# Kernel optimization log

Measured on AMD Instinct MI355X. Metric: run time of the kernel, lower is better.

## Reference

```python
import jax, jax.numpy as jnp
import numpy as np
import math

POOL_OUT = 64  # AdaptiveAvgPool1d output_size


def setup_inputs() -> dict:
    key = jax.random.key(0)
    k1, k2 = jax.random.split(key)
    B, L, C = 8, 4096, 2048
    M, P = 4, 512  # masks per image, num_sample_point
    input_feats = jax.random.normal(k1, (B, L, C), dtype=jnp.float32)
    # normalized (y, x) point coords in [0,1), as produced by m.nonzero()/img_wh
    points_yx = jax.random.uniform(k2, (B, M, P, 2), dtype=jnp.float32)
    return {"input_feats": input_feats, "points_yx": points_yx}


def _point_sample_pool(input_feats, points_yx):
    B, L, C = input_feats.shape
    H = W = int(math.isqrt(L))  # feat.reshape(h, w, c) with h = w = sqrt(L)
    _, M, P, _ = points_yx.shape
    feat = input_feats.reshape(B, H, W, C)

    # point_sample: grid = 2*p - 1, grid_sample align_corners=True =>
    # pixel coord = (grid+1)/2*(dim-1) = p*(dim-1)
    iy = points_yx[..., 0] * (H - 1)  # [B,M,P]
    ix = points_yx[..., 1] * (W - 1)
    y0f = jnp.floor(iy)
    x0f = jnp.floor(ix)
    wy = (iy - y0f)[..., None]  # [B,M,P,1]
    wx = (ix - x0f)[..., None]
    y0 = jnp.clip(y0f.astype(jnp.int32), 0, H - 1)
    x0 = jnp.clip(x0f.astype(jnp.int32), 0, W - 1)
    y1 = jnp.clip(y0 + 1, 0, H - 1)
    x1 = jnp.clip(x0 + 1, 0, W - 1)

    flat = feat.reshape(B, H * W, C)

    def gather(yi, xi):
        idx = (yi * W + xi).reshape(B, M * P)
        return jnp.take_along_axis(flat, idx[..., None], axis=1).reshape(B, M, P, C)

    f00 = gather(y0, x0)
    f01 = gather(y0, x1)
    f10 = gather(y1, x0)
    f11 = gather(y1, x1)
    sampled = (f00 * (1 - wx) + f01 * wx) * (1 - wy) + (f10 * (1 - wx) + f11 * wx) * wy

    # AdaptiveAvgPool1d(output_size=POOL_OUT) over point dim; P % POOL_OUT == 0
    # so it reduces to a chunked mean.
    k = P // POOL_OUT
    pooled = sampled.reshape(B, M, POOL_OUT, k, C).mean(axis=3)
    return pooled  # [B, M, POOL_OUT, C]


def reference(input_feats, points_yx):
    return _point_sample_pool(input_feats, points_yx)
```

## Files before the change

kernel.cpp:

```cpp
#include <hip/hip_runtime.h>

constexpr int Bc    = 8;
constexpr int Lc    = 4096;
constexpr int Cc    = 2048;
constexpr int Mc    = 4;
constexpr int Pc    = 512;
constexpr int POOLc = 64;
constexpr int Kc    = 8;
constexpr int Hc    = 64;
constexpr int Wc    = 64;

__device__ __forceinline__ void fma4(float4& acc, float w, const float4 v) {
    acc.x = fmaf(w, v.x, acc.x);
    acc.y = fmaf(w, v.y, acc.y);
    acc.z = fmaf(w, v.z, acc.z);
    acc.w = fmaf(w, v.w, acc.w);
}

__global__ __launch_bounds__(256) void point_sample_pool_kernel(
    const float* __restrict__ feats,
    const float* __restrict__ pts,
    float* __restrict__ out)
{
    const int blk = blockIdx.x;
    const int o   = blk & (POOLc - 1);
    const int bm  = blk >> 6;
    const int b   = bm >> 2;
    const int tid = threadIdx.x;

    const int cA = tid * 4;
    const int cB = cA + (Cc / 2);

    const float* fb = feats + (size_t)b * Lc * Cc;
    const float* pb = pts + ((size_t)bm * Pc + (size_t)o * Kc) * 2;

    float4 accA = make_float4(0.f, 0.f, 0.f, 0.f);
    float4 accB = make_float4(0.f, 0.f, 0.f, 0.f);

#pragma unroll
    for (int j = 0; j < Kc; ++j) {
        const float py = pb[2 * j + 0];
        const float px = pb[2 * j + 1];
        const float iy = py * (float)(Hc - 1);
        const float ix = px * (float)(Wc - 1);
        const float y0f = floorf(iy);
        const float x0f = floorf(ix);
        const float wy = iy - y0f;
        const float wx = ix - x0f;
        int y0 = (int)y0f; y0 = y0 < 0 ? 0 : (y0 > Hc - 1 ? Hc - 1 : y0);
        int x0 = (int)x0f; x0 = x0 < 0 ? 0 : (x0 > Wc - 1 ? Wc - 1 : x0);
        const int y1 = (y0 + 1 > Hc - 1) ? Hc - 1 : y0 + 1;
        const int x1 = (x0 + 1 > Wc - 1) ? Wc - 1 : x0 + 1;

        const float w00 = (1.f - wx) * (1.f - wy);
        const float w01 = wx * (1.f - wy);
        const float w10 = (1.f - wx) * wy;
        const float w11 = wx * wy;

        const float* r00 = fb + (size_t)(y0 * Wc + x0) * Cc;
        const float* r01 = fb + (size_t)(y0 * Wc + x1) * Cc;
        const float* r10 = fb + (size_t)(y1 * Wc + x0) * Cc;
        const float* r11 = fb + (size_t)(y1 * Wc + x1) * Cc;

        const float4 a00 = *(const float4*)(r00 + cA);
        const float4 b00 = *(const float4*)(r00 + cB);
        const float4 a01 = *(const float4*)(r01 + cA);
        const float4 b01 = *(const float4*)(r01 + cB);
        const float4 a10 = *(const float4*)(r10 + cA);
        const float4 b10 = *(const float4*)(r10 + cB);
        const float4 a11 = *(const float4*)(r11 + cA);
        const float4 b11 = *(const float4*)(r11 + cB);

        fma4(accA, w00, a00); fma4(accB, w00, b00);
        fma4(accA, w01, a01); fma4(accB, w01, b01);
        fma4(accA, w10, a10); fma4(accB, w10, b10);
        fma4(accA, w11, a11); fma4(accB, w11, b11);
    }

    const float inv_k = 1.0f / (float)Kc;
    accA.x *= inv_k; accA.y *= inv_k; accA.z *= inv_k; accA.w *= inv_k;
    accB.x *= inv_k; accB.y *= inv_k; accB.z *= inv_k; accB.w *= inv_k;

    float* ob = out + (size_t)blk * Cc;
    *(float4*)(ob + cA) = accA;
    *(float4*)(ob + cB) = accB;
}

extern "C" void kernel_launch(void* const* d_in, const int* in_sizes, int n_in,
                              void* d_out, int out_size, void* d_ws, size_t ws_size,
                              hipStream_t stream) {
    const float* feats = (const float*)d_in[0];
    const float* pts   = (const float*)d_in[1];
    float* out         = (float*)d_out;

    const int grid = Bc * Mc * POOLc;
    point_sample_pool_kernel<<<grid, 256, 0, stream>>>(feats, pts, out);
}
```

Before: 359.0 us.

## Split channel halves across blocks and precompute bilinear offsets and weights

```diff
diff --git a/kernel.cpp b/kernel.cpp
--- a/kernel.cpp
+++ b/kernel.cpp
@@ -17,32 +17,30 @@
     acc.w = fmaf(w, v.w, acc.w);
 }
 
-__global__ __launch_bounds__(256) void point_sample_pool_kernel(
+__global__ __launch_bounds__(256, 4) void point_sample_pool_kernel(
     const float* __restrict__ feats,
     const float* __restrict__ pts,
     float* __restrict__ out)
 {
-    const int blk = blockIdx.x;
-    const int o   = blk & (POOLc - 1);
-    const int bm  = blk >> 6;
-    const int b   = bm >> 2;
-    const int tid = threadIdx.x;
+    const int blk  = blockIdx.x;
+    const int row  = blk >> 1;
+    const int half = blk & 1;
+    const int o    = row & (POOLc - 1);
+    const int bm   = row >> 6;
+    const int b    = bm >> 2;
+    const int tid  = threadIdx.x;
 
-    const int cA = tid * 4;
-    const int cB = cA + (Cc / 2);
+    const int c = half * (Cc / 2) + tid * 4;
 
     const float* fb = feats + (size_t)b * Lc * Cc;
     const float* pb = pts + ((size_t)bm * Pc + (size_t)o * Kc) * 2;
 
-    float4 accA = make_float4(0.f, 0.f, 0.f, 0.f);
-    float4 accB = make_float4(0.f, 0.f, 0.f, 0.f);
-
+    int   off00[Kc], off01[Kc], off10[Kc], off11[Kc];
+    float w00[Kc], w01[Kc], w10[Kc], w11[Kc];
 #pragma unroll
     for (int j = 0; j < Kc; ++j) {
-        const float py = pb[2 * j + 0];
-        const float px = pb[2 * j + 1];
-        const float iy = py * (float)(Hc - 1);
-        const float ix = px * (float)(Wc - 1);
+        const float iy = pb[2 * j + 0] * (float)(Hc - 1);
+        const float ix = pb[2 * j + 1] * (float)(Wc - 1);
         const float y0f = floorf(iy);
         const float x0f = floorf(ix);
         const float wy = iy - y0f;
@@ -51,39 +49,48 @@
         int x0 = (int)x0f; x0 = x0 < 0 ? 0 : (x0 > Wc - 1 ? Wc - 1 : x0);
         const int y1 = (y0 + 1 > Hc - 1) ? Hc - 1 : y0 + 1;
         const int x1 = (x0 + 1 > Wc - 1) ? Wc - 1 : x0 + 1;
+        off00[j] = (y0 * Wc + x0) * Cc;
+        off01[j] = (y0 * Wc + x1) * Cc;
+        off10[j] = (y1 * Wc + x0) * Cc;
+        off11[j] = (y1 * Wc + x1) * Cc;
+        w00[j] = (1.f - wx) * (1.f - wy);
+        w01[j] = wx * (1.f - wy);
+        w10[j] = (1.f - wx) * wy;
+        w11[j] = wx * wy;
+    }
 
-        const float w00 = (1.f - wx) * (1.f - wy);
-        const float w01 = wx * (1.f - wy);
-        const float w10 = (1.f - wx) * wy;
-        const float w11 = wx * wy;
+    float4 acc0 = make_float4(0.f, 0.f, 0.f, 0.f);
+    float4 acc1 = make_float4(0.f, 0.f, 0.f, 0.f);
 
-        const float* r00 = fb + (size_t)(y0 * Wc + x0) * Cc;
-        const float* r01 = fb + (size_t)(y0 * Wc + x1) * Cc;
-        const float* r10 = fb + (size_t)(y1 * Wc + x0) * Cc;
-        const float* r11 = fb + (size_t)(y1 * Wc + x1) * Cc;
+#pragma unroll 1
+    for (int j = 0; j < Kc; j += 2) {
+        const float4 a00 = *(const float4*)(fb + off00[j] + c);
+        const float4 a01 = *(const float4*)(fb + off01[j] + c);
+        const float4 a10 = *(const float4*)(fb + off10[j] + c);
+        const float4 a11 = *(const float4*)(fb + off11[j] + c);
+        const float4 b00 = *(const float4*)(fb + off00[j + 1] + c);
+        const float4 b01 = *(const float4*)(fb + off01[j + 1] + c);
+        const float4 b10 = *(const float4*)(fb + off10[j + 1] + c);
+        const float4 b11 = *(const float4*)(fb + off11[j + 1] + c);
 
-        const float4 a00 = *(const float4*)(r00 + cA);
-        const float4 b00 = *(const float4*)(r00 + cB);
-        const float4 a01 = *(const float4*)(r01 + cA);
-        const float4 b01 = *(const float4*)(r01 + cB);
-        const float4 a10 = *(const float4*)(r10 + cA);
-        const float4 b10 = *(const float4*)(r10 + cB);
-        const float4 a11 = *(const float4*)(r11 + cA);
-        const float4 b11 = *(const float4*)(r11 + cB);
-
-        fma4(accA, w00, a00); fma4(accB, w00, b00);
-        fma4(accA, w01, a01); fma4(accB, w01, b01);
-        fma4(accA, w10, a10); fma4(accB, w10, b10);
-        fma4(accA, w11, a11); fma4(accB, w11, b11);
+        fma4(acc0, w00[j], a00);
+        fma4(acc0, w01[j], a01);
+        fma4(acc0, w10[j], a10);
+        fma4(acc0, w11[j], a11);
+        fma4(acc1, w00[j + 1], b00);
+        fma4(acc1, w01[j + 1], b01);
+        fma4(acc1, w10[j + 1], b10);
+        fma4(acc1, w11[j + 1], b11);
     }
 
     const float inv_k = 1.0f / (float)Kc;
-    accA.x *= inv_k; accA.y *= inv_k; accA.z *= inv_k; accA.w *= inv_k;
-    accB.x *= inv_k; accB.y *= inv_k; accB.z *= inv_k; accB.w *= inv_k;
+    float4 r;
+    r.x = (acc0.x + acc1.x) * inv_k;
+    r.y = (acc0.y + acc1.y) * inv_k;
+    r.z = (acc0.z + acc1.z) * inv_k;
+    r.w = (acc0.w + acc1.w) * inv_k;
 
-    float* ob = out + (size_t)blk * Cc;
-    *(float4*)(ob + cA) = accA;
-    *(float4*)(ob + cB) = accB;
+    *(float4*)(out + (size_t)row * Cc + c) = r;
 }
 
 extern "C" void kernel_launch(void* const* d_in, const int* in_sizes, int n_in,
@@ -93,6 +100,6 @@
     const float* pts   = (const float*)d_in[1];
     float* out         = (float*)d_out;
 
-    const int grid = Bc * Mc * POOLc;
+    const int grid = 2 * Bc * Mc * POOLc;
     point_sample_pool_kernel<<<grid, 256, 0, stream>>>(feats, pts, out);
 }
```

Measured after the change: 360.5 us. Within noise of the previous version (+0.4%).
